# Performance work log

Measured on AMD Instinct MI355X. Metric: run time of the kernel, lower is better.

The kernel has to match this reference:

```python
import jax, jax.numpy as jnp
import numpy as np

T, H = 2048, 2048            # tokens, hidden_size
NQ, NKV, D = 32, 4, 128      # q heads, kv heads, head_dim
E, K, I, CAP = 64, 8, 768, 512  # experts, top_k, moe_intermediate, per-expert capacity
EPS, THETA = 1e-6, 10000.0


def setup_inputs() -> dict:
    key = jax.random.key(0)
    ks = jax.random.split(key, 10)
    n = lambda k, shp, sc: jax.random.normal(k, shp, jnp.float32) * sc
    return {
        "hidden_states": n(ks[0], (T, H), 1.0),
        "positions": jnp.arange(T, dtype=jnp.int32),
        "wqkv": n(ks[1], (H, (NQ + 2 * NKV) * D), H ** -0.5),
        "wo": n(ks[2], (NQ * D, H), (NQ * D) ** -0.5),
        "q_norm_w": jnp.ones((D,), jnp.float32),
        "k_norm_w": jnp.ones((D,), jnp.float32),
        "ln1_w": jnp.ones((H,), jnp.float32),
        "ln2_w": jnp.ones((H,), jnp.float32),
        "gate_w": n(ks[3], (H, E), H ** -0.5),
        "w_gate": n(ks[4], (E, H, I), H ** -0.5),
        "w_up": n(ks[5], (E, H, I), H ** -0.5),
        "w_down": n(ks[6], (E, I, H), I ** -0.5),
    }


def _rmsnorm(x, w):
    v = jnp.mean(jnp.square(x.astype(jnp.float32)), axis=-1, keepdims=True)
    return (x.astype(jnp.float32) * jax.lax.rsqrt(v + EPS)).astype(x.dtype) * w


def _rope(x, cos, sin):
    # x: [T, heads, D]; neox-style rotate-half over full head_dim
    x1, x2 = x[..., : D // 2], x[..., D // 2:]
    c, s = cos[:, None, :], sin[:, None, :]
    return jnp.concatenate([x1 * c - x2 * s, x2 * c + x1 * s], axis=-1)


def _forward(hidden_states, positions, wqkv, wo, q_norm_w, k_norm_w, ln1_w, ln2_w, gate_w, w_gate, w_up, w_down):
    x = hidden_states
    # ---- input RMSNorm + GQA attention with QK-norm + RoPE ----
    h = _rmsnorm(x, ln1_w)
    qkv = h @ wqkv
    q, k, v = jnp.split(qkv, [NQ * D, NQ * D + NKV * D], axis=-1)
    q = _rmsnorm(q.reshape(T, NQ, D), q_norm_w)
    k = _rmsnorm(k.reshape(T, NKV, D), k_norm_w)
    v = v.reshape(T, NKV, D)
    inv_freq = 1.0 / (THETA ** (jnp.arange(0, D, 2, dtype=jnp.float32) / D))
    ang = positions.astype(jnp.float32)[:, None] * inv_freq  # [T, D/2]
    cos, sin = jnp.cos(ang), jnp.sin(ang)
    q, k = _rope(q, cos, sin), _rope(k, cos, sin)
    rep = NQ // NKV
    kr = jnp.repeat(k, rep, axis=1)  # [T, NQ, D]
    vr = jnp.repeat(v, rep, axis=1)
    scores = jnp.einsum('qhd,khd->hqk', q, kr) * (D ** -0.5)
    causal = jnp.tril(jnp.ones((T, T), bool))
    scores = jnp.where(causal[None], scores, -1e30)
    probs = jax.nn.softmax(scores, axis=-1)
    attn = jnp.einsum('hqk,khd->qhd', probs, vr).reshape(T, NQ * D)
    x = x + attn @ wo
    # ---- post-attn RMSNorm + sparse MoE (softmax top-k routing, renormalized) ----
    h = _rmsnorm(x, ln2_w)
    logits = h @ gate_w
    gate_probs = jax.nn.softmax(logits.astype(jnp.float32), axis=-1)
    topk_w, topk_idx = jax.lax.top_k(gate_probs, K)              # [T, K]
    topk_w = topk_w / jnp.sum(topk_w, axis=-1, keepdims=True)    # norm_topk_prob
    flat_e = topk_idx.reshape(-1)                                # [T*K], row-major
    oh = jax.nn.one_hot(flat_e, E, dtype=jnp.int32)
    pos = jnp.sum(jnp.cumsum(oh, axis=0) * oh, axis=-1) - 1      # slot within expert
    x_rep = jnp.repeat(h, K, axis=0)                             # [T*K, H]
    buf = jnp.zeros((E, CAP, H), h.dtype).at[flat_e, pos].set(x_rep, mode='drop')
    g = jnp.einsum('ech,ehi->eci', buf, w_gate)
    u = jnp.einsum('ech,ehi->eci', buf, w_up)
    act = jax.nn.silu(g) * u
    out_buf = jnp.einsum('eci,eih->ech', act, w_down)
    valid = (pos < CAP).astype(h.dtype)                          # CAP >> expected load; no drops in practice
    gathered = out_buf[flat_e, jnp.clip(pos, 0, CAP - 1)]        # [T*K, H]
    w = topk_w.reshape(-1).astype(h.dtype) * valid
    moe_out = jnp.sum((gathered * w[:, None]).reshape(T, K, H), axis=1)
    return x + moe_out


def reference(hidden_states, positions, wqkv, wo, q_norm_w, k_norm_w, ln1_w, ln2_w, gate_w, w_gate, w_up, w_down):
    return _forward(hidden_states, positions, wqkv, wo, q_norm_w, k_norm_w,
                    ln1_w, ln2_w, gate_w, w_gate, w_up, w_down)
```

## Files before the change

kernel.cpp:

```cpp
#include <hip/hip_runtime.h>
#include <hip/hip_bf16.h>

#define T_    2048
#define H_    2048
#define NQ_   32
#define NKV_  4
#define D_    128
#define E_    64
#define TK_   8
#define I_    768
#define CAP_  512
#define QKVW_ 5120

typedef float  f32x4  __attribute__((ext_vector_type(4)));
typedef __bf16 bf16x8 __attribute__((ext_vector_type(8)));
typedef int    i32x4  __attribute__((ext_vector_type(4)));
#define AS1 __attribute__((address_space(1)))
#define AS3 __attribute__((address_space(3)))

static __device__ __forceinline__ unsigned f2bf_u(float f){
  unsigned u = __builtin_bit_cast(unsigned, f);
  u += 0x7fffu + ((u >> 16) & 1u);
  return u >> 16;
}
static __device__ __forceinline__ float bf2f(unsigned h){
  unsigned u = h << 16;
  return __builtin_bit_cast(float, u);
}
struct HL { int h; int l; };
static __device__ __forceinline__ HL packsplit(float a, float b){
  unsigned ah = f2bf_u(a), bh = f2bf_u(b);
  float al = a - bf2f(ah), bl = b - bf2f(bh);
  HL r;
  r.h = (int)(ah | (bh << 16));
  r.l = (int)(f2bf_u(al) | (f2bf_u(bl) << 16));
  return r;
}
static __device__ __forceinline__ f32x4 mfma16(bf16x8 a, bf16x8 b, f32x4 c){
  return __builtin_amdgcn_mfma_f32_16x16x32_bf16(a, b, c, 0, 0, 0);
}

__global__ __launch_bounds__(256) void k_rms(const float* __restrict__ in,
                                             const float* __restrict__ w,
                                             unsigned short* __restrict__ outh,
                                             unsigned short* __restrict__ outl,
                                             float* __restrict__ cpy)
{
  const int t = blockIdx.x, tid = threadIdx.x;
  const float* row = in + (long)t * H_;
  float4 a = *(const float4*)(row + tid*8);
  float4 b = *(const float4*)(row + tid*8 + 4);
  float ss = a.x*a.x + a.y*a.y + a.z*a.z + a.w*a.w
           + b.x*b.x + b.y*b.y + b.z*b.z + b.w*b.w;
  #pragma unroll
  for (int o = 32; o >= 1; o >>= 1) ss += __shfl_xor(ss, o);
  __shared__ float red[4];
  if ((tid & 63) == 0) red[tid >> 6] = ss;
  __syncthreads();
  float tot = red[0] + red[1] + red[2] + red[3];
  float rs = rsqrtf(tot * (1.0f / (float)H_) + 1e-6f);
  const float* wp = w + tid*8;
  float vv[8] = {a.x, a.y, a.z, a.w, b.x, b.y, b.z, b.w};
  i32x4 oh, ol;
  #pragma unroll
  for (int d = 0; d < 4; d++){
    float v0 = vv[2*d]   * rs * wp[2*d];
    float v1 = vv[2*d+1] * rs * wp[2*d+1];
    HL r = packsplit(v0, v1);
    oh[d] = r.h; ol[d] = r.l;
  }
  *(i32x4*)(outh + (long)t * H_ + tid*8) = oh;
  if (outl) *(i32x4*)(outl + (long)t * H_ + tid*8) = ol;
  if (cpy){
    *(float4*)(cpy + (long)t * H_ + tid*8)     = a;
    *(float4*)(cpy + (long)t * H_ + tid*8 + 4) = b;
  }
}

__global__ __launch_bounds__(64) void k_ropetab(const int* __restrict__ pos,
                                                float* __restrict__ cosb,
                                                float* __restrict__ sinb)
{
  int t = blockIdx.x, j = threadIdx.x;
  float p = (float)pos[t];
  float freq = expf(-(float)j * (2.0f / (float)D_) * 9.210340371976184f);
  float ang = p * freq;
  cosb[t*64 + j] = cosf(ang);
  sinb[t*64 + j] = sinf(ang);
}

__global__ __launch_bounds__(256) void k_qknorm(const float* __restrict__ qkv,
                                                const float* __restrict__ qw,
                                                const float* __restrict__ kw,
                                                const float* __restrict__ cosb,
                                                const float* __restrict__ sinb,
                                                unsigned short* __restrict__ qh,
                                                unsigned short* __restrict__ ql,
                                                unsigned short* __restrict__ khp,
                                                unsigned short* __restrict__ klp)
{
  int gw = blockIdx.x*4 + (threadIdx.x >> 6);
  int lane = threadIdx.x & 63;
  int t = gw / 36, hh = gw - t*36;
  const float* src; const float* w;
  unsigned short *dh, *dl;
  if (hh < NQ_){
    src = qkv + (long)t*QKVW_ + hh*D_;
    w = qw;
    dh = qh + ((long)t*NQ_ + hh)*D_;
    dl = ql + ((long)t*NQ_ + hh)*D_;
  } else {
    int kh = hh - NQ_;
    src = qkv + (long)t*QKVW_ + NQ_*D_ + kh*D_;
    w = kw;
    dh = khp + ((long)t*NKV_ + kh)*D_;
    dl = klp + ((long)t*NKV_ + kh)*D_;
  }
  float a = src[lane], b = src[lane + 64];
  float ss = a*a + b*b;
  #pragma unroll
  for (int o = 32; o >= 1; o >>= 1) ss += __shfl_xor(ss, o);
  float rs = rsqrtf(ss * (1.0f / (float)D_) + 1e-6f);
  a *= rs * w[lane];
  b *= rs * w[lane + 64];
  float c = cosb[t*64 + lane], s = sinb[t*64 + lane];
  float r0 = a*c - b*s;
  float r1 = b*c + a*s;
  unsigned h0 = f2bf_u(r0), h1 = f2bf_u(r1);
  dh[lane]      = (unsigned short)h0;
  dh[lane + 64] = (unsigned short)h1;
  dl[lane]      = (unsigned short)f2bf_u(r0 - bf2f(h0));
  dl[lane + 64] = (unsigned short)f2bf_u(r1 - bf2f(h1));
}

__global__ __launch_bounds__(256) void k_vtrans(const float* __restrict__ qkv,
                                                unsigned short* __restrict__ vth,
                                                unsigned short* __restrict__ vtl)
{
  __shared__ unsigned short tileh[64][136];
  __shared__ unsigned short tilel[64][136];
  const int t0 = blockIdx.x * 64;
  const int hv = blockIdx.y;
  const int tid = threadIdx.x;
  #pragma unroll
  for (int it = 0; it < 8; it++){
    int chunk = tid + it*256;
    int r  = chunk >> 5;
    int c4 = chunk & 31;
    float4 v = *(const float4*)(qkv + (long)(t0 + r)*QKVW_ + (NQ_+NKV_)*D_ + hv*D_ + c4*4);
    float vals[4] = {v.x, v.y, v.z, v.w};
    #pragma unroll
    for (int q = 0; q < 4; q++){
      unsigned hi = f2bf_u(vals[q]);
      tileh[r][c4*4+q] = (unsigned short)hi;
      tilel[r][c4*4+q] = (unsigned short)f2bf_u(vals[q] - bf2f(hi));
    }
  }
  __syncthreads();
  int d = tid >> 1, hf = tid & 1;
  long dbase = ((long)(hv*D_ + d))*T_ + t0 + hf*32;
  #pragma unroll
  for (int k = 0; k < 4; k++){
    i32x4 oh, ol;
    #pragma unroll
    for (int d2 = 0; d2 < 4; d2++){
      int r0 = hf*32 + k*8 + d2*2, r1 = r0 + 1;
      oh[d2] = (int)((unsigned)tileh[r0][d] | ((unsigned)tileh[r1][d] << 16));
      ol[d2] = (int)((unsigned)tilel[r0][d] | ((unsigned)tilel[r1][d] << 16));
    }
    *(i32x4*)(vth + dbase + k*8) = oh;
    *(i32x4*)(vtl + dbase + k*8) = ol;
  }
}

#define VISSUE(G, BUF) { \
  const int kst_ = (G) >> 2, dp_ = (G) & 3; \
  _Pragma("unroll") \
  for (int dd = 0; dd < 2; dd++){ \
    int dn_ = dp_*2 + dd; \
    long voff = ((long)(hk*D_ + dn_*16 + l15))*T_ + kv0 + kst_*32 + g16*8; \
    BUF[dd*2]   = *(const bf16x8*)(vth + voff); \
    BUF[dd*2+1] = *(const bf16x8*)(vtl + voff); \
  } }
#define VPV(G, BUF) { \
  const int kst_ = (G) >> 2, dp_ = (G) & 3; \
  _Pragma("unroll") \
  for (int dd = 0; dd < 2; dd++){ \
    int dn_ = dp_*2 + dd; \
    o[dn_] = mfma16(pah[kst_], BUF[dd*2+1], o[dn_]); \
    o[dn_] = mfma16(pal[kst_], BUF[dd*2],   o[dn_]); \
    o[dn_] = mfma16(pah[kst_], BUF[dd*2],   o[dn_]); \
  } }

__global__ __launch_bounds__(256,2) void k_attn(const unsigned short* __restrict__ qbh,
                                                const unsigned short* __restrict__ qbl,
                                                const unsigned short* __restrict__ kbh,
                                                const unsigned short* __restrict__ kbl,
                                                const unsigned short* __restrict__ vth,
                                                const unsigned short* __restrict__ vtl,
                                                unsigned short* __restrict__ abh,
                                                unsigned short* __restrict__ abl)
{
  __shared__ char ldsK[2][2][16384];
  const int b   = blockIdx.x;
  const int xcd = b & 7, kk = xcd >> 1;
  const int s_  = ((b >> 3) << 1) | (xcd & 1);
  const int h   = kk*8 + (s_ >> 4);
  const int p   = s_ & 15;
  const int hk  = kk;
  const int tid = threadIdx.x;
  const int wv  = tid >> 6, lane = tid & 63;
  const int l15 = lane & 15, g16 = lane >> 4;
  const float sc = 0.08838834764831845f;

  long gb[4];
  #pragma unroll
  for (int i = 0; i < 4; i++){
    int srow = i*16 + (tid >> 4);
    int c = (tid & 15) ^ (srow & 7);
    gb[i] = ((long)srow*NKV_ + hk)*D_ + c*8;
  }

  for (int ph = 0; ph < 2; ph++){
    const int qt  = ph ? p : (31 - p);
    const int q0  = qt*64 + wv*16;
    const int ntB = qt + 1;

    bf16x8 qfh[4], qfl[4];
    {
      long qoff = ((long)(q0 + l15)*NQ_ + h)*D_ + g16*8;
      #pragma unroll
      for (int ks = 0; ks < 4; ks++){
        qfh[ks] = *(const bf16x8*)(qbh + qoff + ks*32);
        qfl[ks] = *(const bf16x8*)(qbl + qoff + ks*32);
      }
    }

    f32x4 zz = {0.f,0.f,0.f,0.f};
    f32x4 o[8];
    #pragma unroll
    for (int dn = 0; dn < 8; dn++) o[dn] = zz;
    float m_run = -1e30f, l_run = 0.f;

    __syncthreads();
    #pragma unroll
    for (int i = 0; i < 4; i++){
      __builtin_amdgcn_global_load_lds((const AS1 int*)(kbh + gb[i]),
          (AS3 int*)((AS3 char*)&ldsK[0][0][0] + i*4096 + tid*16), 16, 0, 0);
      __builtin_amdgcn_global_load_lds((const AS1 int*)(kbl + gb[i]),
          (AS3 int*)((AS3 char*)&ldsK[0][1][0] + i*4096 + tid*16), 16, 0, 0);
    }

    for (int t = 0; t < ntB; t++){
      __syncthreads();
      const int kv0 = t*64;
      if (t+1 < ntB){
        long kadd = (long)(t+1)*64*NKV_*D_;
        int nb = (t+1) & 1;
        #pragma unroll
        for (int i = 0; i < 4; i++){
          __builtin_amdgcn_global_load_lds((const AS1 int*)(kbh + gb[i] + kadd),
              (AS3 int*)((AS3 char*)&ldsK[nb][0][0] + i*4096 + tid*16), 16, 0, 0);
          __builtin_amdgcn_global_load_lds((const AS1 int*)(kbl + gb[i] + kadd),
              (AS3 int*)((AS3 char*)&ldsK[nb][1][0] + i*4096 + tid*16), 16, 0, 0);
        }
      }
      {
        const char* Kh = &ldsK[t & 1][0][0];
        const char* Kl = &ldsK[t & 1][1][0];
        f32x4 sA[4];
        #pragma unroll
        for (int sub = 0; sub < 4; sub++) sA[sub] = zz;
        __builtin_amdgcn_s_setprio(1);
        #pragma unroll
        for (int sub = 0; sub < 4; sub++){
          int row = sub*16 + l15;
          int rsw = (row & 7) << 4;
          #pragma unroll
          for (int ks = 0; ks < 4; ks++){
            bf16x8 kh = *(const bf16x8*)(Kh + row*256 + (((ks*4 + g16)*16) ^ rsw));
            bf16x8 kl = *(const bf16x8*)(Kl + row*256 + (((ks*4 + g16)*16) ^ rsw));
            sA[sub] = mfma16(kh, qfl[ks], sA[sub]);
            sA[sub] = mfma16(kl, qfh[ks], sA[sub]);
            sA[sub] = mfma16(kh, qfh[ks], sA[sub]);
          }
        }
        __builtin_amdgcn_s_setprio(0);
        bf16x8 vA[4], vB[4];
        VISSUE(0, vA);
        {
          int qrow = q0 + l15;
          float mt = -1e30f;
          #pragma unroll
          for (int sub = 0; sub < 4; sub++)
            #pragma unroll
            for (int r = 0; r < 4; r++){
              int kva = kv0 + sub*16 + g16*4 + r;
              float v = sA[sub][r]*sc;
              if (kva > qrow) v = -1e30f;
              sA[sub][r] = v;
              mt = fmaxf(mt, v);
            }
          mt = fmaxf(mt, __shfl_xor(mt,16));
          mt = fmaxf(mt, __shfl_xor(mt,32));
          float mnew = fmaxf(m_run, mt);
          float corr = __expf(m_run - mnew);
          float ps = 0.f;
          #pragma unroll
          for (int sub = 0; sub < 4; sub++)
            #pragma unroll
            for (int r = 0; r < 4; r++){
              float e = __expf(sA[sub][r] - mnew);
              sA[sub][r] = e;
              ps += e;
            }
          ps += __shfl_xor(ps,16);
          ps += __shfl_xor(ps,32);
          l_run = l_run*corr + ps;
          m_run = mnew;
          #pragma unroll
          for (int r = 0; r < 4; r++){
            float cr = __shfl(corr, g16*4 + r);
            #pragma unroll
            for (int dn = 0; dn < 8; dn++) o[dn][r] *= cr;
          }
        }
        bf16x8 pah[2], pal[2];
        #pragma unroll
        for (int kst = 0; kst < 2; kst++){
          f32x4 s0 = sA[2*kst], s1 = sA[2*kst+1];
          i32x4 pkh, pkl;
          #pragma unroll
          for (int d = 0; d < 4; d++){
            const int e0 = 2*d, e1 = 2*d+1;
            int src0 = (((2*g16 + (e0>>2)) & 3) << 4) | l15;
            int src1 = (((2*g16 + (e1>>2)) & 3) << 4) | l15;
            float a0t = __shfl(s0[e0&3], src0), a1t = __shfl(s1[e0&3], src0);
            float b0t = __shfl(s0[e1&3], src1), b1t = __shfl(s1[e1&3], src1);
            float va = (g16 >= 2) ? a1t : a0t;
            float vb = (g16 >= 2) ? b1t : b0t;
            HL r = packsplit(va, vb);
            pkh[d] = r.h; pkl[d] = r.l;
          }
          pah[kst] = __builtin_bit_cast(bf16x8, pkh);
          pal[kst] = __builtin_bit_cast(bf16x8, pkl);
        }
        VISSUE(1, vB);
        __builtin_amdgcn_s_setprio(1);
        VPV(0, vA); VISSUE(2, vA);
        VPV(1, vB); VISSUE(3, vB);
        VPV(2, vA); VISSUE(4, vA);
        VPV(3, vB); VISSUE(5, vB);
        VPV(4, vA); VISSUE(6, vA);
        VPV(5, vB); VISSUE(7, vB);
        VPV(6, vA);
        VPV(7, vB);
        __builtin_amdgcn_s_setprio(0);
      }
    }

    {
      float linv = 1.0f / l_run;
      #pragma unroll
      for (int r = 0; r < 4; r++){
        float lr = __shfl(linv, g16*4 + r);
        long row = q0 + g16*4 + r;
        #pragma unroll
        for (int dn = 0; dn < 8; dn++){
          float v = o[dn][r]*lr;
          unsigned hi = f2bf_u(v);
          long idx = row*(NQ_*D_) + h*D_ + dn*16 + l15;
          abh[idx] = (unsigned short)hi;
          abl[idx] = (unsigned short)f2bf_u(v - bf2f(hi));
        }
      }
    }
  }
}

struct SA {
  const unsigned short* Ah;
  const unsigned short* Al;
  const float* B;
  int lda, ldb, K, ldc;
  float* Cf;
  const float* add;
};

template<int MODE>
__global__ __launch_bounds__(256,2) void k_gs(SA ga)
{
  __shared__ unsigned short ldsAh[128*64];
  __shared__ unsigned short ldsAl[128*64];
  __shared__ unsigned short ldsBh[8*128*8];
  __shared__ unsigned short ldsBl[8*128*8];
  const int tid = threadIdx.x;
  const int lane = tid & 63;
  const int wv = tid >> 6;
  const int wm = (wv >> 1)*64, wn = (wv & 1)*64;
  const int l15 = lane & 15, g16 = lane >> 4;

  const long m0 = (long)blockIdx.y * 128;
  const long n0 = (long)blockIdx.x * 128;

  long aoff[4];
  #pragma unroll
  for (int i = 0; i < 4; i++){
    int chunk = tid + i*256;
    int m = chunk >> 3, c = chunk & 7;
    aoff[i] = (m0 + m) * (long)ga.lda + c*8;
  }
  const float* brow = ga.B + n0 + (long)((tid >> 5)*8) * ga.ldb + (tid & 31)*4;

  f32x4 zz = {0.f,0.f,0.f,0.f};
  f32x4 acc[4][4];
  #pragma unroll
  for (int i = 0; i < 4; i++)
    #pragma unroll
    for (int j = 0; j < 4; j++) acc[i][j] = zz;

  i32x4 pva[4], pvl[4];
  float4 pb[8];
  #pragma unroll
  for (int i = 0; i < 4; i++){
    pva[i] = *(const i32x4*)(ga.Ah + aoff[i]);
    pvl[i] = *(const i32x4*)(ga.Al + aoff[i]);
  }
  #pragma unroll
  for (int r = 0; r < 8; r++) pb[r] = *(const float4*)(brow + (long)r * ga.ldb);

  for (int kt = 0; kt < ga.K; kt += 64){
    __syncthreads();
    #pragma unroll
    for (int i = 0; i < 4; i++){
      int chunk = tid + i*256;
      int m = chunk >> 3, c = chunk & 7;
      int sw = (c*16) ^ ((m & 7) << 4);
      *(i32x4*)((char*)ldsAh + m*128 + sw) = pva[i];
      *(i32x4*)((char*)ldsAl + m*128 + sw) = pvl[i];
    }
    {
      i32x4 ph0, ph1, ph2, ph3, pl0, pl1, pl2, pl3;
      #pragma unroll
      for (int r = 0; r < 8; r += 2){
        float4 va = pb[r];
        float4 vb = pb[r+1];
        int d = r >> 1;
        HL rx = packsplit(va.x, vb.x); ph0[d] = rx.h; pl0[d] = rx.l;
        HL ry = packsplit(va.y, vb.y); ph1[d] = ry.h; pl1[d] = ry.l;
        HL rz = packsplit(va.z, vb.z); ph2[d] = rz.h; pl2[d] = rz.l;
        HL rw = packsplit(va.w, vb.w); ph3[d] = rw.h; pl3[d] = rw.l;
      }
      int kbb = tid >> 5, nb = (tid & 31)*4;
      long bo = ((long)kbb*128 + nb) << 4;
      char* bph = (char*)ldsBh + bo;
      char* bpl = (char*)ldsBl + bo;
      *(i32x4*)(bph)      = ph0;  *(i32x4*)(bpl)      = pl0;
      *(i32x4*)(bph + 16) = ph1;  *(i32x4*)(bpl + 16) = pl1;
      *(i32x4*)(bph + 32) = ph2;  *(i32x4*)(bpl + 32) = pl2;
      *(i32x4*)(bph + 48) = ph3;  *(i32x4*)(bpl + 48) = pl3;
    }
    __syncthreads();
    if (kt + 64 < ga.K){
      #pragma unroll
      for (int i = 0; i < 4; i++){
        pva[i] = *(const i32x4*)(ga.Ah + aoff[i] + kt + 64);
        pvl[i] = *(const i32x4*)(ga.Al + aoff[i] + kt + 64);
      }
      #pragma unroll
      for (int r = 0; r < 8; r++) pb[r] = *(const float4*)(brow + (long)(kt + 64 + r) * ga.ldb);
    }
    #pragma unroll
    for (int ks = 0; ks < 2; ks++){
      bf16x8 afh[4], afl[4], bfh[4], bfl[4];
      #pragma unroll
      for (int i = 0; i < 4; i++){
        int m = wm + i*16 + l15;
        int sw = (ks*64 + g16*16) ^ ((m & 7) << 4);
        afh[i] = *(const bf16x8*)((const char*)ldsAh + m*128 + sw);
        afl[i] = *(const bf16x8*)((const char*)ldsAl + m*128 + sw);
      }
      #pragma unroll
      for (int j = 0; j < 4; j++){
        int n = wn + j*16 + l15;
        long bo = ((long)(ks*4 + g16)*128 + n) << 4;
        bfh[j] = *(const bf16x8*)((const char*)ldsBh + bo);
        bfl[j] = *(const bf16x8*)((const char*)ldsBl + bo);
      }
      #pragma unroll
      for (int i = 0; i < 4; i++)
        #pragma unroll
        for (int j = 0; j < 4; j++){
          acc[i][j] = mfma16(afh[i], bfl[j], acc[i][j]);
          acc[i][j] = mfma16(afl[i], bfh[j], acc[i][j]);
          acc[i][j] = mfma16(afh[i], bfh[j], acc[i][j]);
        }
    }
  }

  #pragma unroll
  for (int i = 0; i < 4; i++){
    #pragma unroll
    for (int j = 0; j < 4; j++){
      #pragma unroll
      for (int r = 0; r < 4; r++){
        float v = acc[i][j][r];
        long grow = m0 + wm + i*16 + g16*4 + r;
        long gcol = n0 + wn + j*16 + l15;
        long idx = grow * ga.ldc + gcol;
        if (MODE == 0) ga.Cf[idx] = v;
        else           ga.Cf[idx] = v + ga.add[idx];
      }
    }
  }
}

struct GA {
  const unsigned short* A;
  const float* B;
  const float* B2;
  int lda, ldb, K, ldc;
  unsigned short* Cb;
  const int* rowidx;
  const float* wslot;
  const int* counts;
  float* outp;
};

template<int MODE>
__global__ __launch_bounds__(256,3) void k_gemm(GA ga)
{
  __shared__ unsigned short ldsA[256*64];
  __shared__ unsigned short ldsB[8*64*8];
  const int tid = threadIdx.x;
  const int lane = tid & 63;
  const int wv = tid >> 6;
  const int l15 = lane & 15, g16 = lane >> 4;

  long m0 = (long)blockIdx.y * 256;
  long n0 = 0;
  const unsigned short* A = ga.A;
  const int* rowmap = nullptr;
  int e = blockIdx.z, count = ga.counts[e];
  if ((int)m0 >= count) return;

  const float* bbase;
  {
    int c2 = (tid & 31) * 2;
    if (MODE == 2){
      n0 = (long)blockIdx.x * 32;
      rowmap = ga.rowidx + e * CAP_;
      if (c2 < 32) bbase = ga.B  + (long)e * H_ * I_ + n0 + c2;
      else         bbase = ga.B2 + (long)e * H_ * I_ + n0 + (c2 - 32);
    } else {
      n0 = (long)blockIdx.x * 64;
      bbase = ga.B + (long)e * I_ * H_ + n0 + c2;
      A = ga.A + (long)e * CAP_ * I_;
    }
  }

  const unsigned short* arow[8];
  #pragma unroll
  for (int i = 0; i < 8; i++){
    int chunk = tid + i*256;
    int m = chunk >> 3, c = chunk & 7;
    int csw = c ^ (m & 7);
    int s = (int)m0 + m; if (s > count - 1) s = count - 1;
    long row = (MODE == 2) ? (long)rowmap[s] : (long)s;
    arow[i] = A + row * (long)ga.lda + csw*8;
  }
  const float* brow = bbase + (long)((tid >> 5)*8) * ga.ldb;

  f32x4 zz = {0.f,0.f,0.f,0.f};
  f32x4 acc[4][4];
  #pragma unroll
  for (int i = 0; i < 4; i++)
    #pragma unroll
    for (int j = 0; j < 4; j++) acc[i][j] = zz;

  float2 pb[8];
  #pragma unroll
  for (int r = 0; r < 8; r++) pb[r] = *(const float2*)(brow + (long)r * ga.ldb);

  for (int kt = 0; kt < ga.K; kt += 64){
    __syncthreads();
    #pragma unroll
    for (int i = 0; i < 8; i++){
      __builtin_amdgcn_global_load_lds((const AS1 int*)(arow[i] + kt),
          (AS3 int*)((AS3 char*)ldsA + i*4096 + tid*16), 16, 0, 0);
    }
    {
      i32x4 p0, p1;
      #pragma unroll
      for (int r = 0; r < 8; r += 2){
        int d = r >> 1;
        p0[d] = (int)(f2bf_u(pb[r].x) | (f2bf_u(pb[r+1].x) << 16));
        p1[d] = (int)(f2bf_u(pb[r].y) | (f2bf_u(pb[r+1].y) << 16));
      }
      int kbb = tid >> 5, nb = (tid & 31)*2;
      char* bp = (char*)ldsB + (((long)kbb*64 + nb) << 4);
      *(i32x4*)(bp)      = p0;
      *(i32x4*)(bp + 16) = p1;
    }
    __syncthreads();
    if (kt + 64 < ga.K){
      #pragma unroll
      for (int r = 0; r < 8; r++) pb[r] = *(const float2*)(brow + (long)(kt + 64 + r) * ga.ldb);
    }
    #pragma unroll
    for (int ks = 0; ks < 2; ks++){
      bf16x8 af[4], bfv[4];
      #pragma unroll
      for (int i = 0; i < 4; i++){
        int m = wv*64 + i*16 + l15;
        af[i] = *(const bf16x8*)((const char*)ldsA + m*128 + ((ks*64 + g16*16) ^ ((m & 7) << 4)));
      }
      #pragma unroll
      for (int j = 0; j < 4; j++){
        int n = j*16 + l15;
        bfv[j] = *(const bf16x8*)((const char*)ldsB + (((long)(ks*4 + g16)*64 + n) << 4));
      }
      #pragma unroll
      for (int i = 0; i < 4; i++)
        #pragma unroll
        for (int j = 0; j < 4; j++)
          acc[i][j] = mfma16(af[i], bfv[j], acc[i][j]);
    }
  }

  if (MODE == 2){
    #pragma unroll
    for (int i = 0; i < 4; i++){
      #pragma unroll
      for (int jj = 0; jj < 2; jj++){
        #pragma unroll
        for (int r = 0; r < 4; r++){
          float g = acc[i][jj][r];
          float u = acc[i][jj+2][r];
          float actv = g / (1.f + __expf(-g)) * u;
          int grow = (int)m0 + wv*64 + i*16 + g16*4 + r;
          if (grow < count)
            ga.Cb[((long)e*CAP_ + grow)*I_ + n0 + jj*16 + l15] = (unsigned short)f2bf_u(actv);
        }
      }
    }
  } else {
    #pragma unroll
    for (int i = 0; i < 4; i++){
      #pragma unroll
      for (int j = 0; j < 4; j++){
        #pragma unroll
        for (int r = 0; r < 4; r++){
          float v = acc[i][j][r];
          int grow = (int)m0 + wv*64 + i*16 + g16*4 + r;
          long gcol = n0 + j*16 + l15;
          if (grow < count){
            float ww = ga.wslot[e*CAP_ + grow];
            int tk = ga.rowidx[e*CAP_ + grow];
            atomicAdd(ga.outp + (long)tk*H_ + gcol, v*ww);
          }
        }
      }
    }
  }
}

__global__ __launch_bounds__(64) void k_router(const float* __restrict__ x2,
                                               const float* __restrict__ ln2w,
                                               const float* __restrict__ gwt,
                                               int* __restrict__ tidx,
                                               float* __restrict__ twv)
{
  __shared__ float hl[H_];
  __shared__ int   ti[8];
  __shared__ float tv[8];
  const int t = blockIdx.x, lane = threadIdx.x;
  const float* row = x2 + (long)t * H_;
  float ss = 0.f;
  #pragma unroll 4
  for (int j = 0; j < 32; j++){
    float v = row[j*64 + lane];
    hl[j*64 + lane] = v;
    ss += v*v;
  }
  #pragma unroll
  for (int o = 32; o >= 1; o >>= 1) ss += __shfl_xor(ss, o);
  float rs = rsqrtf(ss * (1.0f / (float)H_) + 1e-6f);
  __syncthreads();
  #pragma unroll 4
  for (int j = 0; j < 32; j++) hl[j*64 + lane] *= rs * ln2w[j*64 + lane];
  __syncthreads();
  float acc = 0.f;
  #pragma unroll 8
  for (int k = 0; k < H_; k++) acc += hl[k] * gwt[(long)k*E_ + lane];
  float mx = acc;
  #pragma unroll
  for (int o = 32; o >= 1; o >>= 1) mx = fmaxf(mx, __shfl_xor(mx, o));
  float p = __expf(acc - mx);
  float sm = p;
  #pragma unroll
  for (int o = 32; o >= 1; o >>= 1) sm += __shfl_xor(sm, o);
  p /= sm;
  float cur = p, wsum = 0.f;
  #pragma unroll
  for (int j = 0; j < 8; j++){
    float v = cur; int ix = lane;
    #pragma unroll
    for (int o = 1; o < 64; o <<= 1){
      float ov = __shfl_xor(v, o); int oi = __shfl_xor(ix, o);
      if (ov > v || (ov == v && oi < ix)){ v = ov; ix = oi; }
    }
    if (lane == ix) cur = -1.f;
    wsum += v;
    if (lane == 0){ ti[j] = ix; tv[j] = v; }
  }
  __syncthreads();
  if (lane < 8){
    tidx[t*TK_ + lane] = ti[lane];
    twv [t*TK_ + lane] = tv[lane] / wsum;
  }
}

__global__ __launch_bounds__(64) void k_route(const int* __restrict__ tidx,
                                              const float* __restrict__ twv,
                                              int* __restrict__ rowi,
                                              float* __restrict__ wsl,
                                              int* __restrict__ cnts)
{
  const int e = blockIdx.x, lane = threadIdx.x;
  int run = 0;
  for (int s0 = 0; s0 < T_*TK_; s0 += 64){
    int s = s0 + lane;
    int idx = tidx[s];
    bool m = (idx == e);
    unsigned long long mk = __ballot(m);
    int pre = __popcll(mk & ((1ull << lane) - 1ull));
    int pos = run + pre;
    if (m && pos < CAP_){
      rowi[e*CAP_ + pos] = s >> 3;
      wsl [e*CAP_ + pos] = twv[s];
    }
    run += __popcll(mk);
  }
  if (lane == 0) cnts[e] = (run < CAP_) ? run : CAP_;
}

extern "C" void kernel_launch(void* const* d_in, const int* in_sizes, int n_in,
                              void* d_out, int out_size, void* d_ws, size_t ws_size,
                              hipStream_t stream)
{
  (void)in_sizes; (void)n_in; (void)out_size; (void)ws_size;
  const float* x    = (const float*)d_in[0];
  const int*   pos  = (const int*)d_in[1];
  const float* wqkv = (const float*)d_in[2];
  const float* wo   = (const float*)d_in[3];
  const float* qnw  = (const float*)d_in[4];
  const float* knw  = (const float*)d_in[5];
  const float* ln1  = (const float*)d_in[6];
  const float* ln2  = (const float*)d_in[7];
  const float* gwt  = (const float*)d_in[8];
  const float* wg   = (const float*)d_in[9];
  const float* wu   = (const float*)d_in[10];
  const float* wd   = (const float*)d_in[11];
  float* out = (float*)d_out;

  char* ws = (char*)d_ws;
  size_t off = 0;
  auto alloc = [&](size_t b)->void*{ void* p = ws + off; off += (b + 255) & ~(size_t)255; return p; };

  unsigned short* hbh = (unsigned short*)alloc((size_t)T_*H_*2);
  unsigned short* hbl = (unsigned short*)alloc((size_t)T_*H_*2);
  float* qkv          = (float*)alloc((size_t)T_*QKVW_*4);
  float* cosb         = (float*)alloc((size_t)T_*64*4);
  float* sinb         = (float*)alloc((size_t)T_*64*4);
  unsigned short* qbh = (unsigned short*)alloc((size_t)T_*NQ_*D_*2);
  unsigned short* qbl = (unsigned short*)alloc((size_t)T_*NQ_*D_*2);
  unsigned short* kbh = (unsigned short*)alloc((size_t)T_*NKV_*D_*2);
  unsigned short* kbl = (unsigned short*)alloc((size_t)T_*NKV_*D_*2);
  unsigned short* vth = (unsigned short*)alloc((size_t)NKV_*D_*T_*2);
  unsigned short* vtl = (unsigned short*)alloc((size_t)NKV_*D_*T_*2);
  unsigned short* abh = (unsigned short*)alloc((size_t)T_*NQ_*D_*2);
  unsigned short* abl = (unsigned short*)alloc((size_t)T_*NQ_*D_*2);
  float* x2           = (float*)alloc((size_t)T_*H_*4);
  unsigned short* h2b = (unsigned short*)alloc((size_t)T_*H_*2);
  int* tidx           = (int*)alloc((size_t)T_*TK_*4);
  float* twv          = (float*)alloc((size_t)T_*TK_*4);
  int* rowi           = (int*)alloc((size_t)E_*CAP_*4);
  float* wsl          = (float*)alloc((size_t)E_*CAP_*4);
  int* cnts           = (int*)alloc((size_t)E_*4);
  unsigned short* gu  = (unsigned short*)alloc((size_t)E_*CAP_*I_*2);

  k_rms<<<T_, 256, 0, stream>>>(x, ln1, hbh, hbl, nullptr);
  k_ropetab<<<T_, 64, 0, stream>>>(pos, cosb, sinb);
  {
    SA a{}; a.Ah = hbh; a.Al = hbl; a.B = wqkv; a.lda = H_; a.ldb = QKVW_; a.K = H_; a.ldc = QKVW_; a.Cf = qkv;
    k_gs<0><<<dim3(QKVW_/128, T_/128), 256, 0, stream>>>(a);
  }
  k_qknorm<<<T_*36/4, 256, 0, stream>>>(qkv, qnw, knw, cosb, sinb, qbh, qbl, kbh, kbl);
  k_vtrans<<<dim3(T_/64, NKV_), 256, 0, stream>>>(qkv, vth, vtl);
  k_attn<<<512, 256, 0, stream>>>(qbh, qbl, kbh, kbl, vth, vtl, abh, abl);
  {
    SA a{}; a.Ah = abh; a.Al = abl; a.B = wo; a.lda = NQ_*D_; a.ldb = H_; a.K = NQ_*D_; a.ldc = H_;
    a.Cf = x2; a.add = x;
    k_gs<1><<<dim3(H_/128, T_/128), 256, 0, stream>>>(a);
  }
  k_rms<<<T_, 256, 0, stream>>>(x2, ln2, h2b, nullptr, out);
  k_router<<<T_, 64, 0, stream>>>(x2, ln2, gwt, tidx, twv);
  k_route<<<E_, 64, 0, stream>>>(tidx, twv, rowi, wsl, cnts);
  {
    GA a{}; a.A = h2b; a.B = wg; a.B2 = wu; a.lda = H_; a.ldb = I_; a.K = H_;
    a.Cb = gu; a.rowidx = rowi; a.counts = cnts;
    k_gemm<2><<<dim3(24, 2, E_), 256, 0, stream>>>(a);
  }
  {
    GA a{}; a.A = gu; a.B = wd; a.lda = I_; a.ldb = H_; a.K = I_;
    a.counts = cnts; a.rowidx = rowi; a.wslot = wsl; a.outp = out;
    k_gemm<3><<<dim3(32, 2, E_), 256, 0, stream>>>(a);
  }
}
```

Before: 1.479 ms.

## Compute router logits with split-bf16 MFMA GEMM instead of per-token scalar loop

Replaces the per-token router kernel, which used scalar FP32 FMAs to run a 2048x64 dot product per token, with a block-tiled MFMA GEMM over 256-token tiles. It uses hi/lo bf16 splitting (three MFMAs per pair) to keep near-FP32 accuracy. The RMSNorm kernel now also writes the low bf16 half, and a small softmax/top-k kernel reads the logits. This adds an extra logits buffer round trip and a kernel launch, and launches only 8 blocks for the GEMM, which may underutilize the GPU.

```diff
diff --git a/kernel.cpp b/kernel.cpp
--- a/kernel.cpp
+++ b/kernel.cpp
@@ -515,6 +515,144 @@
   }
 }
 
+__global__ __launch_bounds__(256,2) void k_logits(const unsigned short* __restrict__ Ah,
+                                                  const unsigned short* __restrict__ Al,
+                                                  const float* __restrict__ B,
+                                                  float* __restrict__ logits)
+{
+  __shared__ unsigned short ldsAh[256*64];
+  __shared__ unsigned short ldsAl[256*64];
+  __shared__ unsigned short ldsBh[8*64*8];
+  __shared__ unsigned short ldsBl[8*64*8];
+  const int tid = threadIdx.x, lane = tid & 63, wv = tid >> 6;
+  const int l15 = lane & 15, g16 = lane >> 4;
+  const long m0 = (long)blockIdx.x * 256;
+
+  long aoff[8];
+  #pragma unroll
+  for (int i = 0; i < 8; i++){
+    int chunk = tid + i*256;
+    int m = chunk >> 3, c = chunk & 7;
+    int csw = c ^ (m & 7);
+    aoff[i] = (m0 + m) * (long)H_ + csw*8;
+  }
+  const float* brow = B + (long)((tid >> 5)*8) * E_ + (tid & 31)*2;
+
+  f32x4 zz = {0.f,0.f,0.f,0.f};
+  f32x4 acc[4][4];
+  #pragma unroll
+  for (int i = 0; i < 4; i++)
+    #pragma unroll
+    for (int j = 0; j < 4; j++) acc[i][j] = zz;
+
+  float2 pb[8];
+  #pragma unroll
+  for (int r = 0; r < 8; r++) pb[r] = *(const float2*)(brow + (long)r * E_);
+
+  for (int kt = 0; kt < H_; kt += 64){
+    __syncthreads();
+    #pragma unroll
+    for (int i = 0; i < 8; i++){
+      __builtin_amdgcn_global_load_lds((const AS1 int*)(Ah + aoff[i] + kt),
+          (AS3 int*)((AS3 char*)ldsAh + i*4096 + tid*16), 16, 0, 0);
+      __builtin_amdgcn_global_load_lds((const AS1 int*)(Al + aoff[i] + kt),
+          (AS3 int*)((AS3 char*)ldsAl + i*4096 + tid*16), 16, 0, 0);
+    }
+    {
+      i32x4 p0h, p0l, p1h, p1l;
+      #pragma unroll
+      for (int r = 0; r < 8; r += 2){
+        int d = r >> 1;
+        HL rx = packsplit(pb[r].x, pb[r+1].x); p0h[d] = rx.h; p0l[d] = rx.l;
+        HL ry = packsplit(pb[r].y, pb[r+1].y); p1h[d] = ry.h; p1l[d] = ry.l;
+      }
+      int kbb = tid >> 5, nb = (tid & 31)*2;
+      long bo = ((long)kbb*64 + nb) << 4;
+      *(i32x4*)((char*)ldsBh + bo)      = p0h;
+      *(i32x4*)((char*)ldsBh + bo + 16) = p1h;
+      *(i32x4*)((char*)ldsBl + bo)      = p0l;
+      *(i32x4*)((char*)ldsBl + bo + 16) = p1l;
+    }
+    __syncthreads();
+    if (kt + 64 < H_){
+      #pragma unroll
+      for (int r = 0; r < 8; r++) pb[r] = *(const float2*)(brow + (long)(kt + 64 + r) * E_);
+    }
+    #pragma unroll
+    for (int ks = 0; ks < 2; ks++){
+      bf16x8 afh[4], afl[4], bfh[4], bfl[4];
+      #pragma unroll
+      for (int i = 0; i < 4; i++){
+        int m = wv*64 + i*16 + l15;
+        int sw = (ks*64 + g16*16) ^ ((m & 7) << 4);
+        afh[i] = *(const bf16x8*)((const char*)ldsAh + m*128 + sw);
+        afl[i] = *(const bf16x8*)((const char*)ldsAl + m*128 + sw);
+      }
+      #pragma unroll
+      for (int j = 0; j < 4; j++){
+        int n = j*16 + l15;
+        long bo = ((long)(ks*4 + g16)*64 + n) << 4;
+        bfh[j] = *(const bf16x8*)((const char*)ldsBh + bo);
+        bfl[j] = *(const bf16x8*)((const char*)ldsBl + bo);
+      }
+      #pragma unroll
+      for (int i = 0; i < 4; i++)
+        #pragma unroll
+        for (int j = 0; j < 4; j++){
+          acc[i][j] = mfma16(afh[i], bfl[j], acc[i][j]);
+          acc[i][j] = mfma16(afl[i], bfh[j], acc[i][j]);
+          acc[i][j] = mfma16(afh[i], bfh[j], acc[i][j]);
+        }
+    }
+  }
+
+  #pragma unroll
+  for (int i = 0; i < 4; i++)
+    #pragma unroll
+    for (int j = 0; j < 4; j++)
+      #pragma unroll
+      for (int r = 0; r < 4; r++){
+        long row = m0 + wv*64 + i*16 + g16*4 + r;
+        logits[row*E_ + j*16 + l15] = acc[i][j][r];
+      }
+}
+
+__global__ __launch_bounds__(64) void k_router2(const float* __restrict__ logits,
+                                                int* __restrict__ tidx,
+                                                float* __restrict__ twv)
+{
+  __shared__ int   ti[8];
+  __shared__ float tv[8];
+  const int t = blockIdx.x, lane = threadIdx.x;
+  float acc = logits[(long)t*E_ + lane];
+  float mx = acc;
+  #pragma unroll
+  for (int o = 32; o >= 1; o >>= 1) mx = fmaxf(mx, __shfl_xor(mx, o));
+  float p = __expf(acc - mx);
+  float sm = p;
+  #pragma unroll
+  for (int o = 32; o >= 1; o >>= 1) sm += __shfl_xor(sm, o);
+  p /= sm;
+  float cur = p, wsum = 0.f;
+  #pragma unroll
+  for (int j = 0; j < 8; j++){
+    float v = cur; int ix = lane;
+    #pragma unroll
+    for (int o = 1; o < 64; o <<= 1){
+      float ov = __shfl_xor(v, o); int oi = __shfl_xor(ix, o);
+      if (ov > v || (ov == v && oi < ix)){ v = ov; ix = oi; }
+    }
+    if (lane == ix) cur = -1.f;
+    wsum += v;
+    if (lane == 0){ ti[j] = ix; tv[j] = v; }
+  }
+  __syncthreads();
+  if (lane < 8){
+    tidx[t*TK_ + lane] = ti[lane];
+    twv [t*TK_ + lane] = tv[lane] / wsum;
+  }
+}
+
 struct GA {
   const unsigned short* A;
   const float* B;
@@ -662,62 +800,6 @@
         }
       }
     }
-  }
-}
-
-__global__ __launch_bounds__(64) void k_router(const float* __restrict__ x2,
-                                               const float* __restrict__ ln2w,
-                                               const float* __restrict__ gwt,
-                                               int* __restrict__ tidx,
-                                               float* __restrict__ twv)
-{
-  __shared__ float hl[H_];
-  __shared__ int   ti[8];
-  __shared__ float tv[8];
-  const int t = blockIdx.x, lane = threadIdx.x;
-  const float* row = x2 + (long)t * H_;
-  float ss = 0.f;
-  #pragma unroll 4
-  for (int j = 0; j < 32; j++){
-    float v = row[j*64 + lane];
-    hl[j*64 + lane] = v;
-    ss += v*v;
-  }
-  #pragma unroll
-  for (int o = 32; o >= 1; o >>= 1) ss += __shfl_xor(ss, o);
-  float rs = rsqrtf(ss * (1.0f / (float)H_) + 1e-6f);
-  __syncthreads();
-  #pragma unroll 4
-  for (int j = 0; j < 32; j++) hl[j*64 + lane] *= rs * ln2w[j*64 + lane];
-  __syncthreads();
-  float acc = 0.f;
-  #pragma unroll 8
-  for (int k = 0; k < H_; k++) acc += hl[k] * gwt[(long)k*E_ + lane];
-  float mx = acc;
-  #pragma unroll
-  for (int o = 32; o >= 1; o >>= 1) mx = fmaxf(mx, __shfl_xor(mx, o));
-  float p = __expf(acc - mx);
-  float sm = p;
-  #pragma unroll
-  for (int o = 32; o >= 1; o >>= 1) sm += __shfl_xor(sm, o);
-  p /= sm;
-  float cur = p, wsum = 0.f;
-  #pragma unroll
-  for (int j = 0; j < 8; j++){
-    float v = cur; int ix = lane;
-    #pragma unroll
-    for (int o = 1; o < 64; o <<= 1){
-      float ov = __shfl_xor(v, o); int oi = __shfl_xor(ix, o);
-      if (ov > v || (ov == v && oi < ix)){ v = ov; ix = oi; }
-    }
-    if (lane == ix) cur = -1.f;
-    wsum += v;
-    if (lane == 0){ ti[j] = ix; tv[j] = v; }
-  }
-  __syncthreads();
-  if (lane < 8){
-    tidx[t*TK_ + lane] = ti[lane];
-    twv [t*TK_ + lane] = tv[lane] / wsum;
   }
 }
 
@@ -783,6 +865,8 @@
   unsigned short* abl = (unsigned short*)alloc((size_t)T_*NQ_*D_*2);
   float* x2           = (float*)alloc((size_t)T_*H_*4);
   unsigned short* h2b = (unsigned short*)alloc((size_t)T_*H_*2);
+  unsigned short* h2l = (unsigned short*)alloc((size_t)T_*H_*2);
+  float* lgt          = (float*)alloc((size_t)T_*E_*4);
   int* tidx           = (int*)alloc((size_t)T_*TK_*4);
   float* twv          = (float*)alloc((size_t)T_*TK_*4);
   int* rowi           = (int*)alloc((size_t)E_*CAP_*4);
@@ -804,8 +888,9 @@
     a.Cf = x2; a.add = x;
     k_gs<1><<<dim3(H_/128, T_/128), 256, 0, stream>>>(a);
   }
-  k_rms<<<T_, 256, 0, stream>>>(x2, ln2, h2b, nullptr, out);
-  k_router<<<T_, 64, 0, stream>>>(x2, ln2, gwt, tidx, twv);
+  k_rms<<<T_, 256, 0, stream>>>(x2, ln2, h2b, h2l, out);
+  k_logits<<<T_/256, 256, 0, stream>>>(h2b, h2l, gwt, lgt);
+  k_router2<<<T_, 64, 0, stream>>>(lgt, tidx, twv);
   k_route<<<E_, 64, 0, stream>>>(tidx, twv, rowi, wsl, cnts);
   {
     GA a{}; a.A = h2b; a.B = wg; a.B2 = wu; a.lda = H_; a.ldb = I_; a.K = H_;
```

Result: faster. 1.439 ms, median of 3 (-2.7%).
